# Optimization experiments

Measured on AMD Instinct MI355X. Metric: run time of the kernel, lower is better.

The kernel has to match this reference:

```python
import jax, jax.numpy as jnp
import numpy as np

EMBED_DIM = 2048
NUM_HEADS = 16
NUM_KV_GROUPS = 4
HEAD_DIM = EMBED_DIM // NUM_HEADS  # 128


def setup_inputs() -> dict:
    key = jax.random.key(0)
    ks = jax.random.split(key, 9)
    B, S, E = 2, 2048, EMBED_DIM
    kv_dim = HEAD_DIM * NUM_KV_GROUPS
    sc = 1.0 / np.sqrt(E)
    return {
        "x": jax.random.normal(ks[0], (B, S, E), dtype=jnp.float32),
        "Wq": jax.random.normal(ks[1], (E, E), dtype=jnp.float32) * sc,
        "bq": jnp.zeros((E,), dtype=jnp.float32),
        "Wk": jax.random.normal(ks[2], (E, kv_dim), dtype=jnp.float32) * sc,
        "bk": jnp.zeros((kv_dim,), dtype=jnp.float32),
        "Wv": jax.random.normal(ks[3], (E, kv_dim), dtype=jnp.float32) * sc,
        "bv": jnp.zeros((kv_dim,), dtype=jnp.float32),
        "Wo": jax.random.normal(ks[4], (E, E), dtype=jnp.float32) * sc,
        "bo": jnp.zeros((E,), dtype=jnp.float32),
    }


def reference(x, Wq, bq, Wk, bk, Wv, bv, Wo, bo):
    B, S, E = x.shape
    H, G, D = NUM_HEADS, NUM_KV_GROUPS, HEAD_DIM
    R = H // G  # heads per kv group
    # projections
    Q = (x @ Wq + bq).reshape(B, S, H, D).transpose(0, 2, 1, 3)   # [B,H,S,D]
    K = (x @ Wk + bk).reshape(B, S, G, D).transpose(0, 2, 1, 3)   # [B,G,S,D]
    V = (x @ Wv + bv).reshape(B, S, G, D).transpose(0, 2, 1, 3)   # [B,G,S,D]
    # GQA: broadcast KV groups over head subgroups instead of repeat_interleave copy
    Qg = Q.reshape(B, G, R, S, D)
    scores = jnp.einsum('bgrsd,bgtd->bgrst', Qg, K) / np.sqrt(D)  # [B,G,R,S,S]
    weights = jax.nn.softmax(scores, axis=-1)
    out = jnp.einsum('bgrst,bgtd->bgrsd', weights, V)             # [B,G,R,S,D]
    out = out.reshape(B, H, S, D).transpose(0, 2, 1, 3).reshape(B, S, E)
    return out @ Wo + bo
```

## Files before the change

kernel.cpp:

```cpp
#include <hip/hip_runtime.h>
#include <hip/hip_bf16.h>


typedef __attribute__((ext_vector_type(8))) short bf16x8;
typedef __attribute__((ext_vector_type(4))) short bf16x4;
typedef __attribute__((ext_vector_type(4))) float f32x4;

#define MFMA_16x16x32(a, b, c) __builtin_amdgcn_mfma_f32_16x16x32_bf16((a), (b), (c), 0, 0, 0)

__device__ __forceinline__ unsigned short f2bf(float x) {
  union { float f; unsigned int u; } c;
  c.f = x;
  unsigned int u = c.u;
  return (unsigned short)((u + 0x7fffu + ((u >> 16) & 1u)) >> 16);
}

__device__ __forceinline__ void gload_lds16(const void* g, void* l) {
  __builtin_amdgcn_global_load_lds(
      (const __attribute__((address_space(1))) unsigned int*)g,
      (__attribute__((address_space(3))) unsigned int*)l, 16, 0, 0);
}

__global__ void cast_x_kernel(const float* __restrict__ x,
                              unsigned short* __restrict__ out, long n) {
  long i = ((long)blockIdx.x * blockDim.x + threadIdx.x) * 8;
  if (i >= n) return;
  float4 a = *reinterpret_cast<const float4*>(x + i);
  float4 b = *reinterpret_cast<const float4*>(x + i + 4);
  union { unsigned short s[8]; bf16x8 v; } o;
  o.s[0] = f2bf(a.x); o.s[1] = f2bf(a.y); o.s[2] = f2bf(a.z); o.s[3] = f2bf(a.w);
  o.s[4] = f2bf(b.x); o.s[5] = f2bf(b.y); o.s[6] = f2bf(b.z); o.s[7] = f2bf(b.w);
  *reinterpret_cast<bf16x8*>(out + i) = o.v;
}

__global__ void transpose_cast_kernel(const float* __restrict__ src,
                                      unsigned short* __restrict__ dst,
                                      int K, int N) {
  __shared__ float t[32][33];
  const int tx = threadIdx.x, ty = threadIdx.y;
  const int n0 = blockIdx.x * 32, k0 = blockIdx.y * 32;
#pragma unroll
  for (int i = 0; i < 4; i++)
    t[ty + i * 8][tx] = src[(size_t)(k0 + ty + i * 8) * N + n0 + tx];
  __syncthreads();
#pragma unroll
  for (int i = 0; i < 4; i++)
    dst[(size_t)(n0 + ty + i * 8) * K + k0 + tx] = f2bf(t[tx][ty + i * 8]);
}

__global__ void concat_bias_kernel(const float* __restrict__ bq,
                                   const float* __restrict__ bk,
                                   const float* __restrict__ bv,
                                   float* __restrict__ out) {
  int i = blockIdx.x * 256 + threadIdx.x;
  if (i >= 3072) return;
  out[i] = (i < 2048) ? bq[i] : (i < 2560 ? bk[i - 2048] : bv[i - 2560]);
}

__global__ void transpose_v_kernel(const unsigned short* __restrict__ QKV,
                                   unsigned short* __restrict__ Vt) {
  __shared__ unsigned short t[32][33];
  const int tx = threadIdx.x, ty = threadIdx.y;
  const int c0 = blockIdx.x * 32;
  const int r0 = blockIdx.y * 32;
#pragma unroll
  for (int i = 0; i < 4; i++)
    t[ty + i * 8][tx] = QKV[(size_t)(r0 + ty + i * 8) * 3072 + 2560 + c0 + tx];
  __syncthreads();
#pragma unroll
  for (int i = 0; i < 4; i++) {
    const int gd = c0 + ty + i * 8;
    const int r = r0 + tx;
    const int b = r >> 11, s = r & 2047;
    const int sp = (s & ~63) | ((s & 12) << 1) | (((s >> 4) & 1) << 2) | (s & 3) | (s & 32);
    Vt[(size_t)(b * 512 + gd) * 2048 + sp] = t[tx][ty + i * 8];
  }
}

template <int ARNDS, int BRNDS, bool BF16OUT>
__global__ __launch_bounds__(512, 2)
void gemm_pipe_kernel(const unsigned short* __restrict__ A,
                      const unsigned short* __restrict__ Bt,
                      const float* __restrict__ bias,
                      void* __restrict__ C, int M, int N, int K,
                      float qscale, int qcols) {
  constexpr int FM = ARNDS * 4;
  constexpr int FN = BRNDS * 2;
  constexpr int HFM = FM / 2;
  constexpr int BUFE = (ARNDS + BRNDS) * 4096;
  __shared__ unsigned short lds[4 * BUFE];

  const int tid = threadIdx.x;
  const int w = tid >> 6, l = tid & 63, lg = l >> 4, ll = l & 15;
  const int wm = w >> 2, wn = w & 3;
  const int m0 = blockIdx.y * (ARNDS * 128);
  const int n0 = blockIdx.x * (BRNDS * 128);
  const int NT = K >> 5;

  const f32x4 fz = {0.f, 0.f, 0.f, 0.f};
  f32x4 acc[FM][FN];
#pragma unroll
  for (int i = 0; i < FM; i++)
#pragma unroll
    for (int j = 0; j < FN; j++) acc[i][j] = fz;

  const int srow = tid >> 2, schunk = tid & 3;
  const unsigned short* Ag = A + (size_t)(m0 + srow) * K + schunk * 8;
  const unsigned short* Bg = Bt + (size_t)(n0 + srow) * K + schunk * 8;

  auto stageA = [&](int t) {
    unsigned short* dst = &lds[(t & 3) * BUFE + tid * 8];
#pragma unroll
    for (int r = 0; r < ARNDS; ++r)
      gload_lds16(Ag + (size_t)(r * 128) * K + t * 32, dst + r * 4096);
  };
  auto stageB = [&](int t) {
    unsigned short* dst = &lds[(t & 3) * BUFE + ARNDS * 4096 + tid * 8];
#pragma unroll
    for (int r = 0; r < BRNDS; ++r)
      gload_lds16(Bg + (size_t)(r * 128) * K + t * 32, dst + r * 4096);
  };

  stageA(0); stageB(0);
  stageA(1); stageB(1);

  for (int t = 0; t < NT; ++t) {
    if (t + 1 < NT) {
      if constexpr (ARNDS + BRNDS == 4)
        asm volatile("s_waitcnt vmcnt(4)" ::: "memory");
      else
        asm volatile("s_waitcnt vmcnt(3)" ::: "memory");
    } else {
      asm volatile("s_waitcnt vmcnt(0)" ::: "memory");
    }
    __builtin_amdgcn_s_barrier();
    const unsigned short* bufp = &lds[(t & 3) * BUFE];

    bf16x8 bfrag[FN], afrag[HFM];
#pragma unroll
    for (int ni = 0; ni < FN; ++ni)
      bfrag[ni] = *reinterpret_cast<const bf16x8*>(
          &bufp[ARNDS * 4096 + (wn * FN * 16 + ni * 16 + ll) * 32 + lg * 8]);
#pragma unroll
    for (int mi = 0; mi < HFM; ++mi)
      afrag[mi] = *reinterpret_cast<const bf16x8*>(
          &bufp[(wm * FM * 16 + mi * 16 + ll) * 32 + lg * 8]);
    if (t + 2 < NT) stageA(t + 2);
    __builtin_amdgcn_s_setprio(1);
#pragma unroll
    for (int mi = 0; mi < HFM; ++mi)
#pragma unroll
      for (int ni = 0; ni < FN; ++ni)
        acc[mi][ni] = MFMA_16x16x32(afrag[mi], bfrag[ni], acc[mi][ni]);
    __builtin_amdgcn_s_setprio(0);

#pragma unroll
    for (int mi = 0; mi < HFM; ++mi)
      afrag[mi] = *reinterpret_cast<const bf16x8*>(
          &bufp[(wm * FM * 16 + (HFM + mi) * 16 + ll) * 32 + lg * 8]);
    if (t + 2 < NT) stageB(t + 2);
    __builtin_amdgcn_s_setprio(1);
#pragma unroll
    for (int mi = 0; mi < HFM; ++mi)
#pragma unroll
      for (int ni = 0; ni < FN; ++ni)
        acc[HFM + mi][ni] = MFMA_16x16x32(afrag[mi], bfrag[ni], acc[HFM + mi][ni]);
    __builtin_amdgcn_s_setprio(0);
  }

#pragma unroll
  for (int mi = 0; mi < FM; ++mi) {
#pragma unroll
    for (int ni = 0; ni < FN; ++ni) {
      const int gc = n0 + wn * FN * 16 + ni * 16 + ll;
      const float bv = bias[gc];
      const float sc = (gc < qcols) ? qscale : 1.0f;
#pragma unroll
      for (int r = 0; r < 4; ++r) {
        const int gr = m0 + wm * FM * 16 + mi * 16 + 4 * lg + r;
        const float v = (acc[mi][ni][r] + bv) * sc;
        if constexpr (BF16OUT)
          ((unsigned short*)C)[(size_t)gr * N + gc] = f2bf(v);
        else
          ((float*)C)[(size_t)gr * N + gc] = v;
      }
    }
  }
}

__global__ __launch_bounds__(256, 2)
void attn_kernel(const unsigned short* __restrict__ QKV,
                 const unsigned short* __restrict__ Vt,
                 unsigned short* __restrict__ AO) {
  __shared__ unsigned short Klds[64 * 128];
  __shared__ unsigned short Vlds[128 * 64];

  const int tid = threadIdx.x;
  const int w = tid >> 6, l = tid & 63, lg = l >> 4, ll = l & 15;
  const int bh = blockIdx.y;
  const int b = bh >> 4, h = bh & 15, g = h >> 2;
  const int q0 = blockIdx.x * 128 + w * 32;
  const size_t row_base = (size_t)b * 2048 * 3072;
  const unsigned short* Vg = Vt + (size_t)(b * 512 + g * 128) * 2048;

  bf16x8 qf[2][4];
#pragma unroll
  for (int mi = 0; mi < 2; mi++)
#pragma unroll
    for (int ds = 0; ds < 4; ds++)
      qf[mi][ds] = *reinterpret_cast<const bf16x8*>(
          QKV + row_base + (size_t)(q0 + mi * 16 + ll) * 3072 + h * 128 + ds * 32 + 8 * lg);

  const f32x4 fz = {0.f, 0.f, 0.f, 0.f};
  f32x4 o[8][2];
#pragma unroll
  for (int di = 0; di < 8; di++)
#pragma unroll
    for (int mi = 0; mi < 2; mi++) o[di][mi] = fz;
  float m2[2] = {-3.0e38f, -3.0e38f}, lsum[2] = {0.f, 0.f};

  const int krow = tid >> 4, kc8 = tid & 15;
  const int vrow = tid >> 3, vc8 = tid & 7;
  const unsigned short* Kg = QKV + row_base + 2048 + g * 128 + kc8 * 8 + (size_t)krow * 3072;
  int klo[4], vlo[4];
#pragma unroll
  for (int i = 0; i < 4; i++) {
    const int kr = krow + 16 * i;
    klo[i] = (kr * 128 + kc8 * 8) ^ ((kr & 7) << 3);
    const int vr = vrow + 32 * i;
    vlo[i] = (vr * 64 + vc8 * 8) ^ ((vr & 7) << 3);
  }

  bf16x8 kreg[4], vreg[4];
#pragma unroll
  for (int i = 0; i < 4; i++) {
    kreg[i] = *reinterpret_cast<const bf16x8*>(Kg + (size_t)(16 * i) * 3072);
    vreg[i] = *reinterpret_cast<const bf16x8*>(Vg + (size_t)(vrow + 32 * i) * 2048 + vc8 * 8);
  }

  const float THR = 8.0f;

  for (int kt = 0; kt < 32; kt++) {
#pragma unroll
    for (int i = 0; i < 4; i++) *reinterpret_cast<bf16x8*>(&Klds[klo[i]]) = kreg[i];
#pragma unroll
    for (int i = 0; i < 4; i++) *reinterpret_cast<bf16x8*>(&Vlds[vlo[i]]) = vreg[i];
    __syncthreads();

    if (kt + 1 < 32) {
#pragma unroll
      for (int i = 0; i < 4; i++) {
        kreg[i] = *reinterpret_cast<const bf16x8*>(
            Kg + (size_t)((kt + 1) * 64 + 16 * i) * 3072);
        vreg[i] = *reinterpret_cast<const bf16x8*>(
            Vg + (size_t)(vrow + 32 * i) * 2048 + (kt + 1) * 64 + vc8 * 8);
      }
    }

    f32x4 st[4][2];
#pragma unroll
    for (int ni = 0; ni < 4; ni++)
#pragma unroll
      for (int mi = 0; mi < 2; mi++) st[ni][mi] = fz;
#pragma unroll
    for (int ds = 0; ds < 4; ds++) {
      bf16x8 kf[4];
#pragma unroll
      for (int ni = 0; ni < 4; ni++) {
        const int kr = ni * 16 + ll;
        kf[ni] = *reinterpret_cast<const bf16x8*>(
            &Klds[(kr * 128 + ds * 32 + 8 * lg) ^ ((kr & 7) << 3)]);
      }
#pragma unroll
      for (int ni = 0; ni < 4; ni++)
#pragma unroll
        for (int mi = 0; mi < 2; mi++)
          st[ni][mi] = MFMA_16x16x32(kf[ni], qf[mi][ds], st[ni][mi]);
    }

    float pm[2];
#pragma unroll
    for (int mi = 0; mi < 2; mi++) {
      float a0 = fmaxf(fmaxf(st[0][mi][0], st[0][mi][1]), fmaxf(st[0][mi][2], st[0][mi][3]));
      float a1 = fmaxf(fmaxf(st[1][mi][0], st[1][mi][1]), fmaxf(st[1][mi][2], st[1][mi][3]));
      float a2 = fmaxf(fmaxf(st[2][mi][0], st[2][mi][1]), fmaxf(st[2][mi][2], st[2][mi][3]));
      float a3 = fmaxf(fmaxf(st[3][mi][0], st[3][mi][1]), fmaxf(st[3][mi][2], st[3][mi][3]));
      pm[mi] = fmaxf(fmaxf(a0, a1), fmaxf(a2, a3));
      pm[mi] = fmaxf(pm[mi], __shfl_xor(pm[mi], 16, 64));
      pm[mi] = fmaxf(pm[mi], __shfl_xor(pm[mi], 32, 64));
    }
    const bool grow = (pm[0] > m2[0] + THR) || (pm[1] > m2[1] + THR);
    if (__any(grow)) {
#pragma unroll
      for (int mi = 0; mi < 2; mi++) {
        const float mn = fmaxf(m2[mi], pm[mi]);
        const float fac = __builtin_amdgcn_exp2f(m2[mi] - mn);
        m2[mi] = mn;
        lsum[mi] *= fac;
#pragma unroll
        for (int di = 0; di < 8; di++) o[di][mi] *= fac;
      }
    }
    float ps[2] = {0.f, 0.f};
#pragma unroll
    for (int ni = 0; ni < 4; ni++)
#pragma unroll
      for (int mi = 0; mi < 2; mi++)
#pragma unroll
        for (int r = 0; r < 4; r++) {
          const float pv = __builtin_amdgcn_exp2f(st[ni][mi][r] - m2[mi]);
          st[ni][mi][r] = pv;
          ps[mi] += pv;
        }
#pragma unroll
    for (int mi = 0; mi < 2; mi++) {
      ps[mi] += __shfl_xor(ps[mi], 16, 64);
      ps[mi] += __shfl_xor(ps[mi], 32, 64);
      lsum[mi] += ps[mi];
    }

    bf16x8 pf[2][2];
#pragma unroll
    for (int mi = 0; mi < 2; mi++)
#pragma unroll
      for (int ks = 0; ks < 2; ks++)
#pragma unroll
        for (int j = 0; j < 4; j++) {
          pf[mi][ks][j]     = (short)f2bf(st[2 * ks][mi][j]);
          pf[mi][ks][4 + j] = (short)f2bf(st[2 * ks + 1][mi][j]);
        }

#pragma unroll
    for (int ks = 0; ks < 2; ks++)
#pragma unroll
      for (int di = 0; di < 8; di++) {
        const int dr = di * 16 + ll;
        const bf16x8 vf = *reinterpret_cast<const bf16x8*>(
            &Vlds[(dr * 64 + ks * 32 + 8 * lg) ^ ((dr & 7) << 3)]);
#pragma unroll
        for (int mi = 0; mi < 2; mi++)
          o[di][mi] = MFMA_16x16x32(vf, pf[mi][ks], o[di][mi]);
      }
    __syncthreads();
  }

  float invl[2];
#pragma unroll
  for (int mi = 0; mi < 2; mi++) invl[mi] = 1.0f / lsum[mi];
#pragma unroll
  for (int mi = 0; mi < 2; mi++) {
    const size_t rowoff = (size_t)(b * 2048 + q0 + mi * 16 + ll) * 2048 + h * 128;
#pragma unroll
    for (int di = 0; di < 8; di++) {
      union { unsigned short s[4]; bf16x4 v; } ov;
#pragma unroll
      for (int r = 0; r < 4; r++) ov.s[r] = f2bf(o[di][mi][r] * invl[mi]);
      *reinterpret_cast<bf16x4*>(&AO[rowoff + di * 16 + 4 * lg]) = ov.v;
    }
  }
}

extern "C" void kernel_launch(void* const* d_in, const int* in_sizes, int n_in,
                              void* d_out, int out_size, void* d_ws, size_t ws_size,
                              hipStream_t stream) {
  const float* x  = (const float*)d_in[0];
  const float* Wq = (const float*)d_in[1];
  const float* bq = (const float*)d_in[2];
  const float* Wk = (const float*)d_in[3];
  const float* bk = (const float*)d_in[4];
  const float* Wv = (const float*)d_in[5];
  const float* bv = (const float*)d_in[6];
  const float* Wo = (const float*)d_in[7];
  const float* bo = (const float*)d_in[8];
  float* out = (float*)d_out;

  unsigned short* xb    = (unsigned short*)d_ws;
  unsigned short* Vt    = xb;
  unsigned short* WqkvT = xb + (size_t)4096 * 2048;
  unsigned short* WoT   = WqkvT + (size_t)3072 * 2048;
  unsigned short* QKV   = WoT + (size_t)2048 * 2048;
  unsigned short* AO    = QKV + (size_t)4096 * 3072;
  float* bqkv = (float*)(AO + (size_t)4096 * 2048);

  const float QSC2 = 0.08838834764831845f * 1.4426950408889634f;

  cast_x_kernel<<<4096, 256, 0, stream>>>(x, xb, (long)8388608);
  transpose_cast_kernel<<<dim3(64, 64), dim3(32, 8), 0, stream>>>(Wq, WqkvT, 2048, 2048);
  transpose_cast_kernel<<<dim3(16, 64), dim3(32, 8), 0, stream>>>(Wk, WqkvT + (size_t)2048 * 2048, 2048, 512);
  transpose_cast_kernel<<<dim3(16, 64), dim3(32, 8), 0, stream>>>(Wv, WqkvT + (size_t)2560 * 2048, 2048, 512);
  transpose_cast_kernel<<<dim3(64, 64), dim3(32, 8), 0, stream>>>(Wo, WoT, 2048, 2048);
  concat_bias_kernel<<<12, 256, 0, stream>>>(bq, bk, bv, bqkv);

  gemm_pipe_kernel<2, 2, true><<<dim3(12, 16), 512, 0, stream>>>(
      xb, WqkvT, bqkv, QKV, 4096, 3072, 2048, QSC2, 2048);
  transpose_v_kernel<<<dim3(16, 128), dim3(32, 8), 0, stream>>>(QKV, Vt);
  attn_kernel<<<dim3(16, 32), 256, 0, stream>>>(QKV, Vt, AO);
  gemm_pipe_kernel<1, 2, false><<<dim3(8, 32), 512, 0, stream>>>(
      AO, WoT, bo, out, 4096, 2048, 2048, 1.0f, 0);
}
```

Before: 215.5 us.

## Generalize GEMM tiling, fuse weight prep, double-buffer attention LDS, use hardware bf16 cast

Makes the GEMM tile size row-based, so the QKV projection uses a 256x192 tile and launches 256 blocks instead of 192, with a generic unified staging of A and B loads. The four weight transpose-cast launches become one kernel. The attention kernel double-buffers its K and V shared-memory tiles, which removes the trailing barrier per iteration. It also restructures the max reduction and switches the bf16 conversions to the library intrinsic. Together these aim to fill more CUs, cut launch overhead and reduce synchronisation stalls, at the cost of more LDS per attention block and a different LDS footprint for the GEMM.

```diff
diff --git a/kernel.cpp b/kernel.cpp
--- a/kernel.cpp
+++ b/kernel.cpp
@@ -13,6 +13,13 @@
   c.f = x;
   unsigned int u = c.u;
   return (unsigned short)((u + 0x7fffu + ((u >> 16) & 1u)) >> 16);
+}
+
+__device__ __forceinline__ unsigned short f2bf_hw(float x) {
+  __hip_bfloat16 h = __float2bfloat16(x);
+  union { __hip_bfloat16 h; unsigned short u; } c;
+  c.h = h;
+  return c.u;
 }
 
 __device__ __forceinline__ void gload_lds16(const void* g, void* l) {
@@ -33,19 +40,30 @@
   *reinterpret_cast<bf16x8*>(out + i) = o.v;
 }
 
-__global__ void transpose_cast_kernel(const float* __restrict__ src,
-                                      unsigned short* __restrict__ dst,
-                                      int K, int N) {
+__global__ void prep_w_kernel(const float* __restrict__ Wq,
+                              const float* __restrict__ Wk,
+                              const float* __restrict__ Wv,
+                              const float* __restrict__ Wo,
+                              unsigned short* __restrict__ WqkvT,
+                              unsigned short* __restrict__ WoT) {
   __shared__ float t[32][33];
   const int tx = threadIdx.x, ty = threadIdx.y;
-  const int n0 = blockIdx.x * 32, k0 = blockIdx.y * 32;
+  const int ng = blockIdx.x * 32;
+  const int k0 = blockIdx.y * 32;
+  const float* src;
+  int srcN, n0;
+  unsigned short* dst;
+  if (ng < 2048)      { src = Wq; srcN = 2048; n0 = ng;        dst = WqkvT + (size_t)ng * 2048; }
+  else if (ng < 2560) { src = Wk; srcN = 512;  n0 = ng - 2048; dst = WqkvT + (size_t)ng * 2048; }
+  else if (ng < 3072) { src = Wv; srcN = 512;  n0 = ng - 2560; dst = WqkvT + (size_t)ng * 2048; }
+  else                { src = Wo; srcN = 2048; n0 = ng - 3072; dst = WoT + (size_t)(ng - 3072) * 2048; }
 #pragma unroll
   for (int i = 0; i < 4; i++)
-    t[ty + i * 8][tx] = src[(size_t)(k0 + ty + i * 8) * N + n0 + tx];
+    t[ty + i * 8][tx] = src[(size_t)(k0 + ty + i * 8) * srcN + n0 + tx];
   __syncthreads();
 #pragma unroll
   for (int i = 0; i < 4; i++)
-    dst[(size_t)(n0 + ty + i * 8) * K + k0 + tx] = f2bf(t[tx][ty + i * 8]);
+    dst[(size_t)(ty + i * 8) * 2048 + k0 + tx] = f2bf(t[tx][ty + i * 8]);
 }
 
 __global__ void concat_bias_kernel(const float* __restrict__ bq,
@@ -77,24 +95,29 @@
   }
 }
 
-template <int ARNDS, int BRNDS, bool BF16OUT>
+template <int AROWS, int BROWS, bool BF16OUT>
 __global__ __launch_bounds__(512, 2)
 void gemm_pipe_kernel(const unsigned short* __restrict__ A,
                       const unsigned short* __restrict__ Bt,
                       const float* __restrict__ bias,
                       void* __restrict__ C, int M, int N, int K,
                       float qscale, int qcols) {
-  constexpr int FM = ARNDS * 4;
-  constexpr int FN = BRNDS * 2;
+  constexpr int FM = AROWS / 32;
+  constexpr int FN = BROWS / 64;
   constexpr int HFM = FM / 2;
-  constexpr int BUFE = (ARNDS + BRNDS) * 4096;
+  constexpr int TC = (AROWS + BROWS) * 4;
+  constexpr int LOADS = (TC + 511) / 512;
+  constexpr int PC = LOADS * 512;
+  constexpr int BUFE = PC * 8;
+  constexpr int BOFF = AROWS * 32;
+  constexpr int LH = (LOADS + 1) / 2;
   __shared__ unsigned short lds[4 * BUFE];
 
   const int tid = threadIdx.x;
   const int w = tid >> 6, l = tid & 63, lg = l >> 4, ll = l & 15;
   const int wm = w >> 2, wn = w & 3;
-  const int m0 = blockIdx.y * (ARNDS * 128);
-  const int n0 = blockIdx.x * (BRNDS * 128);
+  const int m0 = blockIdx.y * AROWS;
+  const int n0 = blockIdx.x * BROWS;
   const int NT = K >> 5;
 
   const f32x4 fz = {0.f, 0.f, 0.f, 0.f};
@@ -104,32 +127,42 @@
 #pragma unroll
     for (int j = 0; j < FN; j++) acc[i][j] = fz;
 
-  const int srow = tid >> 2, schunk = tid & 3;
-  const unsigned short* Ag = A + (size_t)(m0 + srow) * K + schunk * 8;
-  const unsigned short* Bg = Bt + (size_t)(n0 + srow) * K + schunk * 8;
-
-  auto stageA = [&](int t) {
+  const unsigned short* gsrc[LOADS];
+#pragma unroll
+  for (int i = 0; i < LOADS; ++i) {
+    const int c = tid + 512 * i;
+    if (c < AROWS * 4) {
+      gsrc[i] = A + (size_t)(m0 + (c >> 2)) * K + (c & 3) * 8;
+    } else if (c < TC) {
+      const int cb = c - AROWS * 4;
+      gsrc[i] = Bt + (size_t)(n0 + (cb >> 2)) * K + (cb & 3) * 8;
+    } else {
+      gsrc[i] = Bt + (size_t)n0 * K;
+    }
+  }
+
+  auto stage_lo = [&](int t) {
     unsigned short* dst = &lds[(t & 3) * BUFE + tid * 8];
 #pragma unroll
-    for (int r = 0; r < ARNDS; ++r)
-      gload_lds16(Ag + (size_t)(r * 128) * K + t * 32, dst + r * 4096);
+    for (int i = 0; i < LH; ++i) gload_lds16(gsrc[i] + t * 32, dst + i * 4096);
   };
-  auto stageB = [&](int t) {
-    unsigned short* dst = &lds[(t & 3) * BUFE + ARNDS * 4096 + tid * 8];
-#pragma unroll
-    for (int r = 0; r < BRNDS; ++r)
-      gload_lds16(Bg + (size_t)(r * 128) * K + t * 32, dst + r * 4096);
+  auto stage_hi = [&](int t) {
+    unsigned short* dst = &lds[(t & 3) * BUFE + tid * 8];
+#pragma unroll
+    for (int i = LH; i < LOADS; ++i) gload_lds16(gsrc[i] + t * 32, dst + i * 4096);
   };
 
-  stageA(0); stageB(0);
-  stageA(1); stageB(1);
+  stage_lo(0); stage_hi(0);
+  stage_lo(1); stage_hi(1);
 
   for (int t = 0; t < NT; ++t) {
     if (t + 1 < NT) {
-      if constexpr (ARNDS + BRNDS == 4)
+      if constexpr (LOADS == 4)
         asm volatile("s_waitcnt vmcnt(4)" ::: "memory");
+      else if constexpr (LOADS == 3)
+        asm volatile("s_waitcnt vmcnt(3)" ::: "memory");
       else
-        asm volatile("s_waitcnt vmcnt(3)" ::: "memory");
+        asm volatile("s_waitcnt vmcnt(0)" ::: "memory");
     } else {
       asm volatile("s_waitcnt vmcnt(0)" ::: "memory");
     }
@@ -140,12 +173,12 @@
 #pragma unroll
     for (int ni = 0; ni < FN; ++ni)
       bfrag[ni] = *reinterpret_cast<const bf16x8*>(
-          &bufp[ARNDS * 4096 + (wn * FN * 16 + ni * 16 + ll) * 32 + lg * 8]);
+          &bufp[BOFF + (wn * FN * 16 + ni * 16 + ll) * 32 + lg * 8]);
 #pragma unroll
     for (int mi = 0; mi < HFM; ++mi)
       afrag[mi] = *reinterpret_cast<const bf16x8*>(
-          &bufp[(wm * FM * 16 + mi * 16 + ll) * 32 + lg * 8]);
-    if (t + 2 < NT) stageA(t + 2);
+          &bufp[(wm * (AROWS / 2) + mi * 16 + ll) * 32 + lg * 8]);
+    if (t + 2 < NT) stage_lo(t + 2);
     __builtin_amdgcn_s_setprio(1);
 #pragma unroll
     for (int mi = 0; mi < HFM; ++mi)
@@ -157,8 +190,8 @@
 #pragma unroll
     for (int mi = 0; mi < HFM; ++mi)
       afrag[mi] = *reinterpret_cast<const bf16x8*>(
-          &bufp[(wm * FM * 16 + (HFM + mi) * 16 + ll) * 32 + lg * 8]);
-    if (t + 2 < NT) stageB(t + 2);
+          &bufp[(wm * (AROWS / 2) + (HFM + mi) * 16 + ll) * 32 + lg * 8]);
+    if (t + 2 < NT) stage_hi(t + 2);
     __builtin_amdgcn_s_setprio(1);
 #pragma unroll
     for (int mi = 0; mi < HFM; ++mi)
@@ -177,7 +210,7 @@
       const float sc = (gc < qcols) ? qscale : 1.0f;
 #pragma unroll
       for (int r = 0; r < 4; ++r) {
-        const int gr = m0 + wm * FM * 16 + mi * 16 + 4 * lg + r;
+        const int gr = m0 + wm * (AROWS / 2) + mi * 16 + 4 * lg + r;
         const float v = (acc[mi][ni][r] + bv) * sc;
         if constexpr (BF16OUT)
           ((unsigned short*)C)[(size_t)gr * N + gc] = f2bf(v);
@@ -192,8 +225,8 @@
 void attn_kernel(const unsigned short* __restrict__ QKV,
                  const unsigned short* __restrict__ Vt,
                  unsigned short* __restrict__ AO) {
-  __shared__ unsigned short Klds[64 * 128];
-  __shared__ unsigned short Vlds[128 * 64];
+  __shared__ unsigned short Klds[2][64 * 128];
+  __shared__ unsigned short Vlds[2][128 * 64];
 
   const int tid = threadIdx.x;
   const int w = tid >> 6, l = tid & 63, lg = l >> 4, ll = l & 15;
@@ -241,10 +274,11 @@
   const float THR = 8.0f;
 
   for (int kt = 0; kt < 32; kt++) {
-#pragma unroll
-    for (int i = 0; i < 4; i++) *reinterpret_cast<bf16x8*>(&Klds[klo[i]]) = kreg[i];
-#pragma unroll
-    for (int i = 0; i < 4; i++) *reinterpret_cast<bf16x8*>(&Vlds[vlo[i]]) = vreg[i];
+    const int cb = kt & 1;
+#pragma unroll
+    for (int i = 0; i < 4; i++) *reinterpret_cast<bf16x8*>(&Klds[cb][klo[i]]) = kreg[i];
+#pragma unroll
+    for (int i = 0; i < 4; i++) *reinterpret_cast<bf16x8*>(&Vlds[cb][vlo[i]]) = vreg[i];
     __syncthreads();
 
     if (kt + 1 < 32) {
@@ -269,7 +303,7 @@
       for (int ni = 0; ni < 4; ni++) {
         const int kr = ni * 16 + ll;
         kf[ni] = *reinterpret_cast<const bf16x8*>(
-            &Klds[(kr * 128 + ds * 32 + 8 * lg) ^ ((kr & 7) << 3)]);
+            &Klds[cb][(kr * 128 + ds * 32 + 8 * lg) ^ ((kr & 7) << 3)]);
       }
 #pragma unroll
       for (int ni = 0; ni < 4; ni++)
@@ -281,11 +315,12 @@
     float pm[2];
 #pragma unroll
     for (int mi = 0; mi < 2; mi++) {
-      float a0 = fmaxf(fmaxf(st[0][mi][0], st[0][mi][1]), fmaxf(st[0][mi][2], st[0][mi][3]));
-      float a1 = fmaxf(fmaxf(st[1][mi][0], st[1][mi][1]), fmaxf(st[1][mi][2], st[1][mi][3]));
-      float a2 = fmaxf(fmaxf(st[2][mi][0], st[2][mi][1]), fmaxf(st[2][mi][2], st[2][mi][3]));
-      float a3 = fmaxf(fmaxf(st[3][mi][0], st[3][mi][1]), fmaxf(st[3][mi][2], st[3][mi][3]));
-      pm[mi] = fmaxf(fmaxf(a0, a1), fmaxf(a2, a3));
+      float a0 = fmaxf(fmaxf(st[0][mi][0], st[0][mi][1]), st[0][mi][2]);
+      float a1 = fmaxf(fmaxf(st[0][mi][3], st[1][mi][0]), st[1][mi][1]);
+      float a2 = fmaxf(fmaxf(st[1][mi][2], st[1][mi][3]), st[2][mi][0]);
+      float a3 = fmaxf(fmaxf(st[2][mi][1], st[2][mi][2]), st[2][mi][3]);
+      float a4 = fmaxf(fmaxf(st[3][mi][0], st[3][mi][1]), st[3][mi][2]);
+      pm[mi] = fmaxf(fmaxf(fmaxf(a0, a1), fmaxf(a2, a3)), fmaxf(a4, st[3][mi][3]));
       pm[mi] = fmaxf(pm[mi], __shfl_xor(pm[mi], 16, 64));
       pm[mi] = fmaxf(pm[mi], __shfl_xor(pm[mi], 32, 64));
     }
@@ -326,8 +361,8 @@
       for (int ks = 0; ks < 2; ks++)
 #pragma unroll
         for (int j = 0; j < 4; j++) {
-          pf[mi][ks][j]     = (short)f2bf(st[2 * ks][mi][j]);
-          pf[mi][ks][4 + j] = (short)f2bf(st[2 * ks + 1][mi][j]);
+          pf[mi][ks][j]     = (short)f2bf_hw(st[2 * ks][mi][j]);
+          pf[mi][ks][4 + j] = (short)f2bf_hw(st[2 * ks + 1][mi][j]);
         }
 
 #pragma unroll
@@ -336,12 +371,11 @@
       for (int di = 0; di < 8; di++) {
         const int dr = di * 16 + ll;
         const bf16x8 vf = *reinterpret_cast<const bf16x8*>(
-            &Vlds[(dr * 64 + ks * 32 + 8 * lg) ^ ((dr & 7) << 3)]);
+            &Vlds[cb][(dr * 64 + ks * 32 + 8 * lg) ^ ((dr & 7) << 3)]);
 #pragma unroll
         for (int mi = 0; mi < 2; mi++)
           o[di][mi] = MFMA_16x16x32(vf, pf[mi][ks], o[di][mi]);
       }
-    __syncthreads();
   }
 
   float invl[2];
@@ -354,7 +388,7 @@
     for (int di = 0; di < 8; di++) {
       union { unsigned short s[4]; bf16x4 v; } ov;
 #pragma unroll
-      for (int r = 0; r < 4; r++) ov.s[r] = f2bf(o[di][mi][r] * invl[mi]);
+      for (int r = 0; r < 4; r++) ov.s[r] = f2bf_hw(o[di][mi][r] * invl[mi]);
       *reinterpret_cast<bf16x4*>(&AO[rowoff + di * 16 + 4 * lg]) = ov.v;
     }
   }
@@ -385,16 +419,13 @@
   const float QSC2 = 0.08838834764831845f * 1.4426950408889634f;
 
   cast_x_kernel<<<4096, 256, 0, stream>>>(x, xb, (long)8388608);
-  transpose_cast_kernel<<<dim3(64, 64), dim3(32, 8), 0, stream>>>(Wq, WqkvT, 2048, 2048);
-  transpose_cast_kernel<<<dim3(16, 64), dim3(32, 8), 0, stream>>>(Wk, WqkvT + (size_t)2048 * 2048, 2048, 512);
-  transpose_cast_kernel<<<dim3(16, 64), dim3(32, 8), 0, stream>>>(Wv, WqkvT + (size_t)2560 * 2048, 2048, 512);
-  transpose_cast_kernel<<<dim3(64, 64), dim3(32, 8), 0, stream>>>(Wo, WoT, 2048, 2048);
+  prep_w_kernel<<<dim3(160, 64), dim3(32, 8), 0, stream>>>(Wq, Wk, Wv, Wo, WqkvT, WoT);
   concat_bias_kernel<<<12, 256, 0, stream>>>(bq, bk, bv, bqkv);
 
-  gemm_pipe_kernel<2, 2, true><<<dim3(12, 16), 512, 0, stream>>>(
+  gemm_pipe_kernel<256, 192, true><<<dim3(16, 16), 512, 0, stream>>>(
       xb, WqkvT, bqkv, QKV, 4096, 3072, 2048, QSC2, 2048);
   transpose_v_kernel<<<dim3(16, 128), dim3(32, 8), 0, stream>>>(QKV, Vt);
   attn_kernel<<<dim3(16, 32), 256, 0, stream>>>(QKV, Vt, AO);
-  gemm_pipe_kernel<1, 2, false><<<dim3(8, 32), 512, 0, stream>>>(
+  gemm_pipe_kernel<128, 256, false><<<dim3(8, 32), 512, 0, stream>>>(
       AO, WoT, bo, out, 4096, 2048, 2048, 1.0f, 0);
 }
```

After: 197.9 us. -8.2%, faster.
